# Kernel tuning notes

Measured on AMD Instinct MI355X. Metric: run time of the kernel, lower is better.

The kernel has to match this reference:

```python
import jax, jax.numpy as jnp
import numpy as np

F = 512        # filters (output channels)
C = 512        # input channels
H, W = 256, 256
DENSITY = 26214 / (F * C)  # ~0.1 nonzero fraction (sparsity ~0.9)


def setup_inputs() -> dict:
    key = jax.random.key(0)
    k1, k2, k3, k4 = jax.random.split(key, 4)
    inputs = jax.random.normal(k1, (1, C, H, W), dtype=jnp.float32)
    kernel_vals = jax.random.normal(k2, (F, C), dtype=jnp.float32)
    mask = jax.random.uniform(k3, (F, C)) < DENSITY  # uniform-sparsity connector
    kernel = jnp.where(mask, kernel_vals, 0.0)       # sparse kernel stored dense
    bias = jax.random.normal(k4, (F,), dtype=jnp.float32)
    return {"inputs": inputs, "kernel": kernel, "mask": mask, "bias": bias}


def reference(inputs, kernel, mask, bias):
    # 1x1 conv as spmm: flatten spatial dims -> [C, H*W], sparse kernel [F, C].
    _, c, h, w = inputs.shape
    flat_inputs = inputs.reshape(c, h * w)
    kernel_sp = jnp.where(mask, kernel, 0.0)
    # fused_spmm path: spmm + bias + relu
    flat_output = jax.nn.relu(kernel_sp @ flat_inputs + bias[:, None])
    return flat_output.reshape(1, -1, h, w)
```

## Files before the change

kernel.cpp:

```cpp
#include <hip/hip_runtime.h>
#include <stdint.h>


#define NF 512
#define NC 512
#define HW 65536
#define ELL_CAP 96
#define ELL_STRIDE 104
#define STRIP 64
#define ROWB 128

typedef __fp16 half2_t __attribute__((ext_vector_type(2)));

__global__ __launch_bounds__(256) void prep_ell(const float* __restrict__ kernel,
                                                int2* __restrict__ ell,
                                                int* __restrict__ cnt) {
  const int row = (blockIdx.x * 256 + threadIdx.x) >> 6;
  const int lane = threadIdx.x & 63;
  if (row >= NF) return;
  const float* krow = kernel + (size_t)row * NC;
  int2* erow = ell + (size_t)row * ELL_STRIDE;
  int n = 0;
  for (int step = 0; step < NC / 64; ++step) {
    const int c = step * 64 + lane;
    const float w = krow[c];
    const bool nz = (w != 0.0f);
    const unsigned long long m = __ballot(nz);
    const int pos = n + __popcll(m & ((1ull << lane) - 1ull));
    if (nz && pos < ELL_CAP) erow[pos] = make_int2(c * ROWB, __float_as_int(w));
    n += __popcll(m);
  }
  const int nn = n < ELL_CAP ? n : ELL_CAP;
  for (int p = nn + lane; p < ELL_STRIDE; p += 64) erow[p] = make_int2(0, 0);
  if (lane == 0) cnt[row] = nn;
}

__global__ __launch_bounds__(512) void prep_sort(const int* __restrict__ cnt,
                                                 int* __restrict__ perm,
                                                 int* __restrict__ chunkn) {
  __shared__ int base[ELL_CAP + 1];
  const int tid = threadIdx.x;
  if (tid <= ELL_CAP) base[tid] = 0;
  __syncthreads();
  const int c = cnt[tid];
  atomicAdd(&base[c], 1);
  __syncthreads();
  if (tid == 0) {
    int run = 0;
    for (int k = ELL_CAP; k >= 0; --k) { const int h = base[k]; base[k] = run; run += h; }
  }
  __syncthreads();
  const int rank = atomicAdd(&base[c], 1);
  perm[rank] = tid;
  __syncthreads();
  if (tid < NF / 8) chunkn[tid] = cnt[perm[tid * 8]];
}

__global__ __launch_bounds__(1024, 8) void spmm_main(
    const float* __restrict__ X, const int2* __restrict__ ell,
    const int* __restrict__ perm, const int* __restrict__ chunkn,
    const float* __restrict__ bias, float* __restrict__ out) {
  __shared__ __align__(16) char ldsb[NC * ROWB];

  const int tid = threadIdx.x;
  const int wave = tid >> 6;
  const int lane = tid & 63;
  const int hw0 = blockIdx.x * STRIP;

  {
    const int rsub = lane >> 4;
    const int colf = (lane & 15) * 4;
    for (int i = 0; i < 8; ++i) {
      const int r = wave * 32 + i * 4 + rsub;
      const float4 x4 = *(const float4*)(X + (size_t)r * HW + hw0 + colf);
      const half2_t p0 = __builtin_amdgcn_cvt_pkrtz(x4.x, x4.y);
      const half2_t p1 = __builtin_amdgcn_cvt_pkrtz(x4.z, x4.w);
      uint2 p;
      p.x = __builtin_bit_cast(uint32_t, p0);
      p.y = __builtin_bit_cast(uint32_t, p1);
      *(uint2*)(ldsb + r * ROWB + colf * 2) = p;
    }
  }
  __syncthreads();

  const int l8 = lane & 7;
  const int g = lane >> 3;
  const int lbase = l8 * 16;

  for (int fi = 0; fi < 4; ++fi) {
    const int chunk = fi * 16 + wave;
    const int f = perm[chunk * 8 + g];
    const int n = chunkn[chunk];
    const int quads = (n + 3) >> 2;
    const int4* e4 = (const int4*)(ell + (size_t)f * ELL_STRIDE);
    int4 pA = e4[0], pB = e4[1];
    float a0 = 0.f, a1 = 0.f, a2 = 0.f, a3 = 0.f;
    float a4 = 0.f, a5 = 0.f, a6 = 0.f, a7 = 0.f;

#define PROC(OFF, WB)                                                    \
    {                                                                    \
      const uint4 u = *(const uint4*)(ldsb + (OFF) + lbase);             \
      const float w = __int_as_float(WB);                                \
      const half2_t h0 = __builtin_bit_cast(half2_t, u.x);               \
      const half2_t h1 = __builtin_bit_cast(half2_t, u.y);               \
      const half2_t h2 = __builtin_bit_cast(half2_t, u.z);               \
      const half2_t h3 = __builtin_bit_cast(half2_t, u.w);               \
      a0 = fmaf(w, (float)h0.x, a0); a1 = fmaf(w, (float)h0.y, a1);      \
      a2 = fmaf(w, (float)h1.x, a2); a3 = fmaf(w, (float)h1.y, a3);      \
      a4 = fmaf(w, (float)h2.x, a4); a5 = fmaf(w, (float)h2.y, a5);      \
      a6 = fmaf(w, (float)h3.x, a6); a7 = fmaf(w, (float)h3.y, a7);      \
    }

    for (int q = 0; q < quads; ++q) {
      const int4 cA = pA, cB = pB;
      pA = e4[q * 2 + 2];
      pB = e4[q * 2 + 3];
      PROC(cA.x, cA.y);
      PROC(cA.z, cA.w);
      PROC(cB.x, cB.y);
      PROC(cB.z, cB.w);
    }
#undef PROC

    const float b = bias[f];
    float4 o0, o1;
    o0.x = fmaxf(a0 + b, 0.f); o0.y = fmaxf(a1 + b, 0.f);
    o0.z = fmaxf(a2 + b, 0.f); o0.w = fmaxf(a3 + b, 0.f);
    o1.x = fmaxf(a4 + b, 0.f); o1.y = fmaxf(a5 + b, 0.f);
    o1.z = fmaxf(a6 + b, 0.f); o1.w = fmaxf(a7 + b, 0.f);
    float* op = out + (size_t)f * HW + hw0 + l8 * 8;
    *(float4*)op = o0;
    *(float4*)(op + 4) = o1;
  }
}

extern "C" void kernel_launch(void* const* d_in, const int* in_sizes, int n_in,
                              void* d_out, int out_size, void* d_ws, size_t ws_size,
                              hipStream_t stream) {
  const float* X = (const float*)d_in[0];
  const float* kern = (const float*)d_in[1];
  const float* bias = (const float*)d_in[3];
  float* out = (float*)d_out;

  char* ws = (char*)d_ws;
  int2* ell = (int2*)ws;
  int* cnt = (int*)(ws + (size_t)NF * ELL_STRIDE * 8);
  int* perm = cnt + NF;
  int* chunkn = perm + NF;

  prep_ell<<<NF * 64 / 256, 256, 0, stream>>>(kern, ell, cnt);
  prep_sort<<<1, 512, 0, stream>>>(cnt, perm, chunkn);
  spmm_main<<<HW / STRIP, 1024, 0, stream>>>(X, ell, perm, chunkn, bias, out);
}
```

Baseline: 318.5 us.

## Replace ELL sparse kernel with dense fp16 MFMA GEMM

```diff
diff --git a/kernel.cpp b/kernel.cpp
--- a/kernel.cpp
+++ b/kernel.cpp
@@ -5,132 +5,95 @@
 #define NF 512
 #define NC 512
 #define HW 65536
-#define ELL_CAP 96
-#define ELL_STRIDE 104
-#define STRIP 64
-#define ROWB 128
+#define BN 64
 
-typedef __fp16 half2_t __attribute__((ext_vector_type(2)));
+typedef _Float16 f16x8 __attribute__((ext_vector_type(8)));
+typedef _Float16 f16x4 __attribute__((ext_vector_type(4)));
+typedef float f32x4 __attribute__((ext_vector_type(4)));
 
-__global__ __launch_bounds__(256) void prep_ell(const float* __restrict__ kernel,
-                                                int2* __restrict__ ell,
-                                                int* __restrict__ cnt) {
-  const int row = (blockIdx.x * 256 + threadIdx.x) >> 6;
-  const int lane = threadIdx.x & 63;
-  if (row >= NF) return;
-  const float* krow = kernel + (size_t)row * NC;
-  int2* erow = ell + (size_t)row * ELL_STRIDE;
-  int n = 0;
-  for (int step = 0; step < NC / 64; ++step) {
-    const int c = step * 64 + lane;
-    const float w = krow[c];
-    const bool nz = (w != 0.0f);
-    const unsigned long long m = __ballot(nz);
-    const int pos = n + __popcll(m & ((1ull << lane) - 1ull));
-    if (nz && pos < ELL_CAP) erow[pos] = make_int2(c * ROWB, __float_as_int(w));
-    n += __popcll(m);
-  }
-  const int nn = n < ELL_CAP ? n : ELL_CAP;
-  for (int p = nn + lane; p < ELL_STRIDE; p += 64) erow[p] = make_int2(0, 0);
-  if (lane == 0) cnt[row] = nn;
+__global__ __launch_bounds__(256) void prep_w(const float* __restrict__ kern,
+                                              _Float16* __restrict__ wh) {
+  const int i = blockIdx.x * 256 + threadIdx.x;
+  const float4 v = ((const float4*)kern)[i];
+  f16x4 o;
+  o[0] = (_Float16)v.x;
+  o[1] = (_Float16)v.y;
+  o[2] = (_Float16)v.z;
+  o[3] = (_Float16)v.w;
+  ((f16x4*)wh)[i] = o;
 }
 
-__global__ __launch_bounds__(512) void prep_sort(const int* __restrict__ cnt,
-                                                 int* __restrict__ perm,
-                                                 int* __restrict__ chunkn) {
-  __shared__ int base[ELL_CAP + 1];
-  const int tid = threadIdx.x;
-  if (tid <= ELL_CAP) base[tid] = 0;
-  __syncthreads();
-  const int c = cnt[tid];
-  atomicAdd(&base[c], 1);
-  __syncthreads();
-  if (tid == 0) {
-    int run = 0;
-    for (int k = ELL_CAP; k >= 0; --k) { const int h = base[k]; base[k] = run; run += h; }
-  }
-  __syncthreads();
-  const int rank = atomicAdd(&base[c], 1);
-  perm[rank] = tid;
-  __syncthreads();
-  if (tid < NF / 8) chunkn[tid] = cnt[perm[tid * 8]];
-}
-
-__global__ __launch_bounds__(1024, 8) void spmm_main(
-    const float* __restrict__ X, const int2* __restrict__ ell,
-    const int* __restrict__ perm, const int* __restrict__ chunkn,
+__global__ __launch_bounds__(512, 4) void spmm_mfma(
+    const float* __restrict__ X, const _Float16* __restrict__ Wh,
     const float* __restrict__ bias, float* __restrict__ out) {
-  __shared__ __align__(16) char ldsb[NC * ROWB];
+  __shared__ __align__(16) _Float16 xt[BN * NC];
 
   const int tid = threadIdx.x;
   const int wave = tid >> 6;
   const int lane = tid & 63;
-  const int hw0 = blockIdx.x * STRIP;
+  const int hw0 = blockIdx.x * BN;
 
   {
-    const int rsub = lane >> 4;
-    const int colf = (lane & 15) * 4;
-    for (int i = 0; i < 8; ++i) {
-      const int r = wave * 32 + i * 4 + rsub;
-      const float4 x4 = *(const float4*)(X + (size_t)r * HW + hw0 + colf);
-      const half2_t p0 = __builtin_amdgcn_cvt_pkrtz(x4.x, x4.y);
-      const half2_t p1 = __builtin_amdgcn_cvt_pkrtz(x4.z, x4.w);
-      uint2 p;
-      p.x = __builtin_bit_cast(uint32_t, p0);
-      p.y = __builtin_bit_cast(uint32_t, p1);
-      *(uint2*)(ldsb + r * ROWB + colf * 2) = p;
+    const float* xp = X + hw0 + lane;
+    char* rowb = (char*)xt + lane * (NC * 2);
+    const int xr = lane & 31;
+#pragma unroll
+    for (int j = 0; j < 8; ++j) {
+      const int c0 = wave * 64 + j * 8;
+      f16x8 p;
+#pragma unroll
+      for (int u = 0; u < 8; ++u) p[u] = (_Float16)xp[(size_t)(c0 + u) * HW];
+      *(f16x8*)(rowb + ((((c0 >> 3) ^ xr)) << 4)) = p;
     }
   }
   __syncthreads();
 
-  const int l8 = lane & 7;
-  const int g = lane >> 3;
-  const int lbase = l8 * 16;
+  const int ln = lane & 15;
+  const int l4 = lane >> 4;
+  const int mrow0 = wave * 64;
 
-  for (int fi = 0; fi < 4; ++fi) {
-    const int chunk = fi * 16 + wave;
-    const int f = perm[chunk * 8 + g];
-    const int n = chunkn[chunk];
-    const int quads = (n + 3) >> 2;
-    const int4* e4 = (const int4*)(ell + (size_t)f * ELL_STRIDE);
-    int4 pA = e4[0], pB = e4[1];
-    float a0 = 0.f, a1 = 0.f, a2 = 0.f, a3 = 0.f;
-    float a4 = 0.f, a5 = 0.f, a6 = 0.f, a7 = 0.f;
+  const _Float16* aptr = Wh + (size_t)(mrow0 + ln) * NC + l4 * 8;
 
-#define PROC(OFF, WB)                                                    \
-    {                                                                    \
-      const uint4 u = *(const uint4*)(ldsb + (OFF) + lbase);             \
-      const float w = __int_as_float(WB);                                \
-      const half2_t h0 = __builtin_bit_cast(half2_t, u.x);               \
-      const half2_t h1 = __builtin_bit_cast(half2_t, u.y);               \
-      const half2_t h2 = __builtin_bit_cast(half2_t, u.z);               \
-      const half2_t h3 = __builtin_bit_cast(half2_t, u.w);               \
-      a0 = fmaf(w, (float)h0.x, a0); a1 = fmaf(w, (float)h0.y, a1);      \
-      a2 = fmaf(w, (float)h1.x, a2); a3 = fmaf(w, (float)h1.y, a3);      \
-      a4 = fmaf(w, (float)h2.x, a4); a5 = fmaf(w, (float)h2.y, a5);      \
-      a6 = fmaf(w, (float)h3.x, a6); a7 = fmaf(w, (float)h3.y, a7);      \
+  int bbase[4], bxor[4];
+#pragma unroll
+  for (int nt = 0; nt < 4; ++nt) {
+    const int n = nt * 16 + ln;
+    bbase[nt] = n * (NC * 2);
+    bxor[nt] = n & 31;
+  }
+
+  f32x4 acc[4][4] = {};
+
+#pragma unroll 2
+  for (int ks = 0; ks < 16; ++ks) {
+    f16x8 a[4], b[4];
+#pragma unroll
+    for (int mt = 0; mt < 4; ++mt)
+      a[mt] = *(const f16x8*)(aptr + (size_t)mt * 16 * NC + ks * 32);
+#pragma unroll
+    for (int nt = 0; nt < 4; ++nt) {
+      const int slot = (ks * 4 + l4) ^ bxor[nt];
+      b[nt] = *(const f16x8*)((char*)xt + bbase[nt] + (slot << 4));
     }
+#pragma unroll
+    for (int nt = 0; nt < 4; ++nt)
+#pragma unroll
+      for (int mt = 0; mt < 4; ++mt)
+        acc[mt][nt] = __builtin_amdgcn_mfma_f32_16x16x32_f16(
+            a[mt], b[nt], acc[mt][nt], 0, 0, 0);
+  }
 
-    for (int q = 0; q < quads; ++q) {
-      const int4 cA = pA, cB = pB;
-      pA = e4[q * 2 + 2];
-      pB = e4[q * 2 + 3];
-      PROC(cA.x, cA.y);
-      PROC(cA.z, cA.w);
-      PROC(cB.x, cB.y);
-      PROC(cB.z, cB.w);
+#pragma unroll
+  for (int mt = 0; mt < 4; ++mt) {
+#pragma unroll
+    for (int r = 0; r < 4; ++r) {
+      const int f = mrow0 + mt * 16 + l4 * 4 + r;
+      const float bv = bias[f];
+      float* op = out + (size_t)f * HW + hw0 + ln;
+#pragma unroll
+      for (int nt = 0; nt < 4; ++nt)
+        op[nt * 16] = fmaxf(acc[mt][nt][r] + bv, 0.f);
     }
-#undef PROC
-
-    const float b = bias[f];
-    float4 o0, o1;
-    o0.x = fmaxf(a0 + b, 0.f); o0.y = fmaxf(a1 + b, 0.f);
-    o0.z = fmaxf(a2 + b, 0.f); o0.w = fmaxf(a3 + b, 0.f);
-    o1.x = fmaxf(a4 + b, 0.f); o1.y = fmaxf(a5 + b, 0.f);
-    o1.z = fmaxf(a6 + b, 0.f); o1.w = fmaxf(a7 + b, 0.f);
-    float* op = out + (size_t)f * HW + hw0 + l8 * 8;
-    *(float4*)op = o0;
-    *(float4*)(op + 4) = o1;
   }
 }
 
@@ -142,13 +105,8 @@
   const float* bias = (const float*)d_in[3];
   float* out = (float*)d_out;
 
-  char* ws = (char*)d_ws;
-  int2* ell = (int2*)ws;
-  int* cnt = (int*)(ws + (size_t)NF * ELL_STRIDE * 8);
-  int* perm = cnt + NF;
-  int* chunkn = perm + NF;
+  _Float16* wh = (_Float16*)d_ws;
 
-  prep_ell<<<NF * 64 / 256, 256, 0, stream>>>(kern, ell, cnt);
-  prep_sort<<<1, 512, 0, stream>>>(cnt, perm, chunkn);
-  spmm_main<<<HW / STRIP, 1024, 0, stream>>>(X, ell, perm, chunkn, bias, out);
+  prep_w<<<NF * NC / 4 / 256, 256, 0, stream>>>(kern, wh);
+  spmm_mfma<<<HW / BN, 512, 0, stream>>>(X, wh, bias, out);
 }
```

Measured after the change: 286.9 us. -9.9%, faster.
